# Optimization experiments

Hardware: AMD Instinct MI355X
Metric: run time of the kernel (lower is better)

The kernel has to match this reference:

```python
import jax, jax.numpy as jnp
import numpy as np

N, ID, OD, M, S, L = 65536, 16, 8, 1024, 8, 64


def setup_inputs() -> dict:
    key = jax.random.key(0)
    k1, k2, k3, k4, k5, k6 = jax.random.split(key, 6)
    return {
        "x": jax.random.normal(k1, (N, ID), dtype=jnp.float32),
        "inducing_locations": jax.random.uniform(k2, (M, ID), dtype=jnp.float32),
        "inducing_weights": jax.random.normal(k3, (S, OD, M), dtype=jnp.float32),
        "prior_frequency": jax.random.normal(k4, (OD, ID, L), dtype=jnp.float32),
        "prior_phase": jax.random.uniform(k5, (OD, L), dtype=jnp.float32, maxval=2 * np.pi),
        "prior_weights": jax.random.normal(k6, (S, OD, L), dtype=jnp.float32),
    }


def _rbf_matrix(x, z):
    # ExponentiatedQuadratic with amplitude=1, length_scale=1:
    # k(x,z) = exp(-0.5 * ||x - z||^2)
    x2 = jnp.sum(x * x, axis=-1)[:, None]          # [N,1]
    z2 = jnp.sum(z * z, axis=-1)[None, :]          # [1,M]
    sq = jnp.maximum(x2 + z2 - 2.0 * (x @ z.T), 0.0)
    return jnp.exp(-0.5 * sq)                      # [N,M]


def reference(x, inducing_locations, inducing_weights, prior_frequency, prior_phase, prior_weights):
    # ---- prior (random Fourier features) ----
    # spectral_weights for unit RBF: outer_weights = ones((OD,L)), inner_weights = ones((ID,))
    # rescaled_x = x / 1 = x
    # basis_fn_inner_prod: [OD, N, L]
    inner = jnp.einsum('ni,oil->onl', x, prior_frequency)
    basis_fn = jnp.cos(inner + prior_phase[:, None, :])              # [OD,N,L]
    basis_weight = jnp.sqrt(2.0 / prior_frequency.shape[-1]) * prior_weights  # [S,OD,L]
    f_prior = jnp.einsum('onl,sol->son', basis_fn, basis_weight)     # [S,OD,N]

    # ---- data term (kernel matrix + matvec) ----
    K = _rbf_matrix(x, inducing_locations)                           # [N,M]
    f_data = jnp.einsum('nm,som->son', K, inducing_weights)          # [S,OD,N]

    return f_prior + f_data
```

## Files before the change

kernel.cpp:

```cpp
#include <hip/hip_runtime.h>
#include <hip/hip_bf16.h>

#define N_PTS 65536
#define LOG2E 1.4426950408889634f
#define INV2PI 0.15915494309189535f

typedef __attribute__((ext_vector_type(8))) short short8;
typedef __attribute__((ext_vector_type(4))) short short4v;
typedef __attribute__((ext_vector_type(4))) float float4v;

#if __has_builtin(__builtin_amdgcn_exp2f)
#define EXP2F(x) __builtin_amdgcn_exp2f(x)
#else
#define EXP2F(x) exp2f(x)
#endif

#if __has_builtin(__builtin_amdgcn_cosf) && __has_builtin(__builtin_amdgcn_fractf)
#define COSR(x) __builtin_amdgcn_cosf(__builtin_amdgcn_fractf(x))
#else
#define COSR(x) __cosf((x) * 6.283185307179586f)
#endif

__device__ __forceinline__ short f2b(float f) {
    __hip_bfloat16 h = __float2bfloat16(f);
    return *(short*)&h;
}
__device__ __forceinline__ float b2f(short s) {
    __hip_bfloat16 h = *(__hip_bfloat16*)&s;
    return __bfloat162float(h);
}

#if __has_builtin(__builtin_amdgcn_mfma_f32_16x16x16bf16_1k)
#define HAVE_MFMA16 1
typedef short4v pafrag;
__device__ __forceinline__ float4v pmfma(pafrag a, pafrag b, float4v c) {
    return __builtin_amdgcn_mfma_f32_16x16x16bf16_1k(a, b, c, 0, 0, 0);
}
#else
#define HAVE_MFMA16 0
typedef short8 pafrag;
__device__ __forceinline__ float4v pmfma(pafrag a, pafrag b, float4v c) {
    return __builtin_amdgcn_mfma_f32_16x16x32_bf16(a, b, c, 0, 0, 0);
}
#endif

__device__ __forceinline__ pafrag ldrow(const short* base, int row16, int q, int c) {
#if HAVE_MFMA16
    return *(const pafrag*)(base + (size_t)(row16 + c) * 16 + 4 * q);
#else
    pafrag v = (pafrag)0;
    if (q < 2) v = *(const pafrag*)(base + (size_t)(row16 + c) * 16 + 8 * q);
    return v;
#endif
}
__device__ __forceinline__ pafrag mkxfrag(const float* x, size_t row, int q) {
#if HAVE_MFMA16
    float4v v = *(const float4v*)(x + row * 16 + 4 * q);
    pafrag a;
    a[0] = f2b(v.x); a[1] = f2b(v.y); a[2] = f2b(v.z); a[3] = f2b(v.w);
    return a;
#else
    pafrag a = (pafrag)0;
    if (q < 2) {
        const float4v* xp = (const float4v*)(x + row * 16 + 8 * q);
        float4v v0 = xp[0], v1 = xp[1];
        a[0] = f2b(v0.x); a[1] = f2b(v0.y); a[2] = f2b(v0.z); a[3] = f2b(v0.w);
        a[4] = f2b(v1.x); a[5] = f2b(v1.y); a[6] = f2b(v1.z); a[7] = f2b(v1.w);
    }
    return a;
#endif
}

__device__ __forceinline__ int permrow(int p) {
    return ((p & 12) << 1) + (p & 3) + ((p >> 4) << 2);
}

__global__ __launch_bounds__(256) void prep_kernel(
    const float* __restrict__ z, const float* __restrict__ W,
    const float* __restrict__ F, const float* __restrict__ pw,
    const float* __restrict__ ph,
    short* __restrict__ zb, short* __restrict__ FbB,
    short* __restrict__ BWd, short* __restrict__ Wtb,
    float* __restrict__ nz2P, float* __restrict__ phP)
{
    int t = blockIdx.x * 256 + threadIdx.x;
    if (t < 16384) {
        int row = t >> 4, i = t & 15;
        int src = (row & ~31) + permrow(row & 31);
        zb[t] = f2b(LOG2E * z[src * 16 + i]);
    } else if (t < 17408) {
        int m = t - 16384;
        int src = (m & ~31) + permrow(m & 31);
        const float4v* zp = (const float4v*)(z + (size_t)src * 16);
        float s = 0.f;
        #pragma unroll
        for (int k = 0; k < 4; k++) {
            float4v v = zp[k];
            float a0 = b2f(f2b(v.x)), a1 = b2f(f2b(v.y));
            float a2 = b2f(f2b(v.z)), a3 = b2f(f2b(v.w));
            s += a0 * a0 + a1 * a1 + a2 * a2 + a3 * a3;
        }
        nz2P[m] = -(0.5f * LOG2E * s);
    } else if (t < 25600) {
        int p = t - 17408;
        int row = p >> 4, i = p & 15;
        int srow = (row & ~31) + permrow(row & 31);
        int o = srow >> 6, l = srow & 63;
        FbB[p] = f2b(INV2PI * F[o * 1024 + i * 64 + l]);
    } else if (t < 58368) {
        int p = t - 25600;
        int so = p >> 9, ol = p & 511, o = ol >> 6;
        float v = ((so & 7) == o) ? 0.17677669529663687f * pw[so * 64 + (ol & 63)] : 0.f;
        BWd[p] = f2b(v);
    } else if (t < 123904) {
        int p = t - 58368;
        Wtb[p] = f2b(W[p]);
    } else {
        int j = t - 123904;
        int sj = (j & ~31) + permrow(j & 31);
        phP[j] = INV2PI * ph[sj];
    }
}

__global__ __launch_bounds__(256, 4) void fused_kernel(
    const float* __restrict__ x,
    const short* __restrict__ zb, const short* __restrict__ FbB,
    const short* __restrict__ BWd, const short* __restrict__ Wtb,
    const float* __restrict__ nz2P, const float* __restrict__ phP,
    float* __restrict__ out)
{
    __shared__ float x2c[64];
    __shared__ __align__(16) float rbufA[64 * 68];
    __shared__ __align__(16) float rbufB[64 * 68];

    const int tid = threadIdx.x;
    const int lane = tid & 63, w = tid >> 6;
    const int q = lane >> 4, c = lane & 15;
    const int n0 = blockIdx.x * 64;

    if (tid < 64) {
        float s = 0.f;
        const float4v* xr = (const float4v*)(x + (size_t)(n0 + tid) * 16);
        #pragma unroll
        for (int k = 0; k < 4; k++) {
            float4v v = xr[k];
            float a0 = b2f(f2b(v.x)), a1 = b2f(f2b(v.y));
            float a2 = b2f(f2b(v.z)), a3 = b2f(f2b(v.w));
            s += a0 * a0 + a1 * a1 + a2 * a2 + a3 * a3;
        }
        x2c[tid] = 0.5f * LOG2E * s;
    }

    pafrag ax[4];
    #pragma unroll
    for (int nt = 0; nt < 4; nt++)
        ax[nt] = mkxfrag(x, (size_t)(n0 + nt * 16 + c), q);

    float4v acc[4][4];
    #pragma unroll
    for (int a = 0; a < 4; a++)
        #pragma unroll
        for (int nt = 0; nt < 4; nt++) acc[a][nt] = (float4v)(0.f);

    __syncthreads();

    const int mbase = w * 256;
    #pragma unroll 2
    for (int mb = 0; mb < 8; mb++) {
        const int m0 = mbase + mb * 32;
        pafrag bzA = ldrow(zb, m0, q, c);
        pafrag bzB = ldrow(zb, m0 + 16, q, c);
        float4v c0A = *(const float4v*)(nz2P + m0 + 4 * q);
        float4v c0B = *(const float4v*)(nz2P + m0 + 16 + 4 * q);
        short8 aw0 = *(const short8*)(Wtb + (size_t)(0 * 16 + c) * 1024 + m0 + q * 8);
        short8 aw1 = *(const short8*)(Wtb + (size_t)(1 * 16 + c) * 1024 + m0 + q * 8);
        short8 aw2 = *(const short8*)(Wtb + (size_t)(2 * 16 + c) * 1024 + m0 + q * 8);
        short8 aw3 = *(const short8*)(Wtb + (size_t)(3 * 16 + c) * 1024 + m0 + q * 8);
        #pragma unroll
        for (int nt = 0; nt < 4; nt++) {
            float4v dA = pmfma(bzA, ax[nt], c0A);
            float4v dB = pmfma(bzB, ax[nt], c0B);
            short8 pb;
            pb[0] = f2b(EXP2F(dA[0])); pb[1] = f2b(EXP2F(dA[1]));
            pb[2] = f2b(EXP2F(dA[2])); pb[3] = f2b(EXP2F(dA[3]));
            pb[4] = f2b(EXP2F(dB[0])); pb[5] = f2b(EXP2F(dB[1]));
            pb[6] = f2b(EXP2F(dB[2])); pb[7] = f2b(EXP2F(dB[3]));
            acc[0][nt] = __builtin_amdgcn_mfma_f32_16x16x32_bf16(aw0, pb, acc[0][nt], 0, 0, 0);
            acc[1][nt] = __builtin_amdgcn_mfma_f32_16x16x32_bf16(aw1, pb, acc[1][nt], 0, 0, 0);
            acc[2][nt] = __builtin_amdgcn_mfma_f32_16x16x32_bf16(aw2, pb, acc[2][nt], 0, 0, 0);
            acc[3][nt] = __builtin_amdgcn_mfma_f32_16x16x32_bf16(aw3, pb, acc[3][nt], 0, 0, 0);
        }
    }

    #pragma unroll
    for (int nt = 0; nt < 4; nt++) {
        float sxv = EXP2F(-x2c[nt * 16 + c]);
        #pragma unroll
        for (int a = 0; a < 4; a++) acc[a][nt] *= sxv;
    }

    const int lbase = w * 128;
    #pragma unroll 2
    for (int lb = 0; lb < 4; lb++) {
        const int l0 = lbase + lb * 32;
        pafrag bfA = ldrow(FbB, l0, q, c);
        pafrag bfB = ldrow(FbB, l0 + 16, q, c);
        float4v c0A = *(const float4v*)(phP + l0 + 4 * q);
        float4v c0B = *(const float4v*)(phP + l0 + 16 + 4 * q);
        short8 aw0 = *(const short8*)(BWd + (size_t)(0 * 16 + c) * 512 + l0 + q * 8);
        short8 aw1 = *(const short8*)(BWd + (size_t)(1 * 16 + c) * 512 + l0 + q * 8);
        short8 aw2 = *(const short8*)(BWd + (size_t)(2 * 16 + c) * 512 + l0 + q * 8);
        short8 aw3 = *(const short8*)(BWd + (size_t)(3 * 16 + c) * 512 + l0 + q * 8);
        #pragma unroll
        for (int nt = 0; nt < 4; nt++) {
            float4v dA = pmfma(bfA, ax[nt], c0A);
            float4v dB = pmfma(bfB, ax[nt], c0B);
            short8 pb;
            pb[0] = f2b(COSR(dA[0])); pb[1] = f2b(COSR(dA[1]));
            pb[2] = f2b(COSR(dA[2])); pb[3] = f2b(COSR(dA[3]));
            pb[4] = f2b(COSR(dB[0])); pb[5] = f2b(COSR(dB[1]));
            pb[6] = f2b(COSR(dB[2])); pb[7] = f2b(COSR(dB[3]));
            acc[0][nt] = __builtin_amdgcn_mfma_f32_16x16x32_bf16(aw0, pb, acc[0][nt], 0, 0, 0);
            acc[1][nt] = __builtin_amdgcn_mfma_f32_16x16x32_bf16(aw1, pb, acc[1][nt], 0, 0, 0);
            acc[2][nt] = __builtin_amdgcn_mfma_f32_16x16x32_bf16(aw2, pb, acc[2][nt], 0, 0, 0);
            acc[3][nt] = __builtin_amdgcn_mfma_f32_16x16x32_bf16(aw3, pb, acc[3][nt], 0, 0, 0);
        }
    }

    __syncthreads();
    if (w & 1) {
        float* rb = (w == 1) ? rbufA : rbufB;
        #pragma unroll
        for (int a = 0; a < 4; a++)
            #pragma unroll
            for (int nt = 0; nt < 4; nt++)
                #pragma unroll
                for (int r = 0; r < 4; r++)
                    rb[(a * 16 + 4 * q + r) * 68 + nt * 16 + c] = acc[a][nt][r];
    }
    __syncthreads();
    if (!(w & 1)) {
        float* rb = (w == 0) ? rbufA : rbufB;
        #pragma unroll
        for (int a = 0; a < 4; a++)
            #pragma unroll
            for (int nt = 0; nt < 4; nt++)
                #pragma unroll
                for (int r = 0; r < 4; r++) {
                    int idx = (a * 16 + 4 * q + r) * 68 + nt * 16 + c;
                    rb[idx] += acc[a][nt][r];
                }
    }
    __syncthreads();
    #pragma unroll
    for (int k = 0; k < 16; k++) {
        int idx = k * 256 + tid;
        int row = idx >> 6, nn = idx & 63;
        out[(size_t)row * N_PTS + n0 + nn] = rbufA[row * 68 + nn] + rbufB[row * 68 + nn];
    }
}

extern "C" void kernel_launch(void* const* d_in, const int* in_sizes, int n_in,
                              void* d_out, int out_size, void* d_ws, size_t ws_size,
                              hipStream_t stream) {
    const float* x  = (const float*)d_in[0];
    const float* z  = (const float*)d_in[1];
    const float* W  = (const float*)d_in[2];
    const float* F  = (const float*)d_in[3];
    const float* ph = (const float*)d_in[4];
    const float* pw = (const float*)d_in[5];
    float* out = (float*)d_out;

    char* ws = (char*)d_ws;
    short* zb   = (short*)(ws);
    short* FbB  = (short*)(ws + 32768);
    short* BWd  = (short*)(ws + 49152);
    short* Wtb  = (short*)(ws + 114688);
    float* nz2P = (float*)(ws + 245760);
    float* phP  = (float*)(ws + 249856);

    prep_kernel<<<486, 256, 0, stream>>>(z, W, F, pw, ph, zb, FbB, BWd, Wtb, nz2P, phP);
    fused_kernel<<<1024, 256, 0, stream>>>(x, zb, FbB, BWd, Wtb, nz2P, phP, out);
}
```

Baseline: 107.5 us.

## Give each wave its own 16 points over the full M and L range

Before, four waves shared 64 points and split the M/L reduction, then combined partial sums through LDS. Now each wave of a 128-thread block owns 16 points and loops over all of M and L. That removes the LDS reduction and its barriers, and it writes output straight from registers. It also swaps the bf16 conversion for a manual pack with round-half-up. In exchange, each wave reloads the weight fragments four times as often per point, does less MFMA work per load, and the output stores become less coalesced.

```diff
diff --git a/kernel.cpp b/kernel.cpp
--- a/kernel.cpp
+++ b/kernel.cpp
@@ -8,6 +8,7 @@
 typedef __attribute__((ext_vector_type(8))) short short8;
 typedef __attribute__((ext_vector_type(4))) short short4v;
 typedef __attribute__((ext_vector_type(4))) float float4v;
+typedef __attribute__((ext_vector_type(4))) unsigned int uint4v;
 
 #if __has_builtin(__builtin_amdgcn_exp2f)
 #define EXP2F(x) __builtin_amdgcn_exp2f(x)
@@ -28,6 +29,12 @@
 __device__ __forceinline__ float b2f(short s) {
     __hip_bfloat16 h = *(__hip_bfloat16*)&s;
     return __bfloat162float(h);
+}
+
+__device__ __forceinline__ unsigned int pkbf(float a, float b) {
+    unsigned int ua = __builtin_bit_cast(unsigned int, a) + 0x8000u;
+    unsigned int ub = __builtin_bit_cast(unsigned int, b) + 0x8000u;
+    return (ua >> 16) | (ub & 0xFFFF0000u);
 }
 
 #if __has_builtin(__builtin_amdgcn_mfma_f32_16x16x16bf16_1k)
@@ -122,23 +129,22 @@
     }
 }
 
-__global__ __launch_bounds__(256, 4) void fused_kernel(
+__global__ __launch_bounds__(128, 5) void fused_kernel(
     const float* __restrict__ x,
     const short* __restrict__ zb, const short* __restrict__ FbB,
     const short* __restrict__ BWd, const short* __restrict__ Wtb,
     const float* __restrict__ nz2P, const float* __restrict__ phP,
     float* __restrict__ out)
 {
-    __shared__ float x2c[64];
-    __shared__ __align__(16) float rbufA[64 * 68];
-    __shared__ __align__(16) float rbufB[64 * 68];
+    __shared__ float x2c[32];
 
     const int tid = threadIdx.x;
     const int lane = tid & 63, w = tid >> 6;
     const int q = lane >> 4, c = lane & 15;
-    const int n0 = blockIdx.x * 64;
-
-    if (tid < 64) {
+    const int n0 = blockIdx.x * 32;
+    const int nw = n0 + w * 16;
+
+    if (tid < 32) {
         float s = 0.f;
         const float4v* xr = (const float4v*)(x + (size_t)(n0 + tid) * 16);
         #pragma unroll
@@ -151,23 +157,17 @@
         x2c[tid] = 0.5f * LOG2E * s;
     }
 
-    pafrag ax[4];
+    pafrag ax = mkxfrag(x, (size_t)(nw + c), q);
+
+    float4v acc[4];
     #pragma unroll
-    for (int nt = 0; nt < 4; nt++)
-        ax[nt] = mkxfrag(x, (size_t)(n0 + nt * 16 + c), q);
-
-    float4v acc[4][4];
-    #pragma unroll
-    for (int a = 0; a < 4; a++)
-        #pragma unroll
-        for (int nt = 0; nt < 4; nt++) acc[a][nt] = (float4v)(0.f);
+    for (int a = 0; a < 4; a++) acc[a] = (float4v)(0.f);
 
     __syncthreads();
 
-    const int mbase = w * 256;
     #pragma unroll 2
-    for (int mb = 0; mb < 8; mb++) {
-        const int m0 = mbase + mb * 32;
+    for (int mb = 0; mb < 32; mb++) {
+        const int m0 = mb * 32;
         pafrag bzA = ldrow(zb, m0, q, c);
         pafrag bzB = ldrow(zb, m0 + 16, q, c);
         float4v c0A = *(const float4v*)(nz2P + m0 + 4 * q);
@@ -176,33 +176,29 @@
         short8 aw1 = *(const short8*)(Wtb + (size_t)(1 * 16 + c) * 1024 + m0 + q * 8);
         short8 aw2 = *(const short8*)(Wtb + (size_t)(2 * 16 + c) * 1024 + m0 + q * 8);
         short8 aw3 = *(const short8*)(Wtb + (size_t)(3 * 16 + c) * 1024 + m0 + q * 8);
-        #pragma unroll
-        for (int nt = 0; nt < 4; nt++) {
-            float4v dA = pmfma(bzA, ax[nt], c0A);
-            float4v dB = pmfma(bzB, ax[nt], c0B);
-            short8 pb;
-            pb[0] = f2b(EXP2F(dA[0])); pb[1] = f2b(EXP2F(dA[1]));
-            pb[2] = f2b(EXP2F(dA[2])); pb[3] = f2b(EXP2F(dA[3]));
-            pb[4] = f2b(EXP2F(dB[0])); pb[5] = f2b(EXP2F(dB[1]));
-            pb[6] = f2b(EXP2F(dB[2])); pb[7] = f2b(EXP2F(dB[3]));
-            acc[0][nt] = __builtin_amdgcn_mfma_f32_16x16x32_bf16(aw0, pb, acc[0][nt], 0, 0, 0);
-            acc[1][nt] = __builtin_amdgcn_mfma_f32_16x16x32_bf16(aw1, pb, acc[1][nt], 0, 0, 0);
-            acc[2][nt] = __builtin_amdgcn_mfma_f32_16x16x32_bf16(aw2, pb, acc[2][nt], 0, 0, 0);
-            acc[3][nt] = __builtin_amdgcn_mfma_f32_16x16x32_bf16(aw3, pb, acc[3][nt], 0, 0, 0);
-        }
-    }
-
-    #pragma unroll
-    for (int nt = 0; nt < 4; nt++) {
-        float sxv = EXP2F(-x2c[nt * 16 + c]);
-        #pragma unroll
-        for (int a = 0; a < 4; a++) acc[a][nt] *= sxv;
-    }
-
-    const int lbase = w * 128;
+        float4v dA = pmfma(bzA, ax, c0A);
+        float4v dB = pmfma(bzB, ax, c0B);
+        uint4v u;
+        u[0] = pkbf(EXP2F(dA[0]), EXP2F(dA[1]));
+        u[1] = pkbf(EXP2F(dA[2]), EXP2F(dA[3]));
+        u[2] = pkbf(EXP2F(dB[0]), EXP2F(dB[1]));
+        u[3] = pkbf(EXP2F(dB[2]), EXP2F(dB[3]));
+        short8 pb = __builtin_bit_cast(short8, u);
+        acc[0] = __builtin_amdgcn_mfma_f32_16x16x32_bf16(aw0, pb, acc[0], 0, 0, 0);
+        acc[1] = __builtin_amdgcn_mfma_f32_16x16x32_bf16(aw1, pb, acc[1], 0, 0, 0);
+        acc[2] = __builtin_amdgcn_mfma_f32_16x16x32_bf16(aw2, pb, acc[2], 0, 0, 0);
+        acc[3] = __builtin_amdgcn_mfma_f32_16x16x32_bf16(aw3, pb, acc[3], 0, 0, 0);
+    }
+
+    {
+        float sxv = EXP2F(-x2c[w * 16 + c]);
+        #pragma unroll
+        for (int a = 0; a < 4; a++) acc[a] *= sxv;
+    }
+
     #pragma unroll 2
-    for (int lb = 0; lb < 4; lb++) {
-        const int l0 = lbase + lb * 32;
+    for (int lb = 0; lb < 16; lb++) {
+        const int l0 = lb * 32;
         pafrag bfA = ldrow(FbB, l0, q, c);
         pafrag bfB = ldrow(FbB, l0 + 16, q, c);
         float4v c0A = *(const float4v*)(phP + l0 + 4 * q);
@@ -211,52 +207,26 @@
         short8 aw1 = *(const short8*)(BWd + (size_t)(1 * 16 + c) * 512 + l0 + q * 8);
         short8 aw2 = *(const short8*)(BWd + (size_t)(2 * 16 + c) * 512 + l0 + q * 8);
         short8 aw3 = *(const short8*)(BWd + (size_t)(3 * 16 + c) * 512 + l0 + q * 8);
-        #pragma unroll
-        for (int nt = 0; nt < 4; nt++) {
-            float4v dA = pmfma(bfA, ax[nt], c0A);
-            float4v dB = pmfma(bfB, ax[nt], c0B);
-            short8 pb;
-            pb[0] = f2b(COSR(dA[0])); pb[1] = f2b(COSR(dA[1]));
-            pb[2] = f2b(COSR(dA[2])); pb[3] = f2b(COSR(dA[3]));
-            pb[4] = f2b(COSR(dB[0])); pb[5] = f2b(COSR(dB[1]));
-            pb[6] = f2b(COSR(dB[2])); pb[7] = f2b(COSR(dB[3]));
-            acc[0][nt] = __builtin_amdgcn_mfma_f32_16x16x32_bf16(aw0, pb, acc[0][nt], 0, 0, 0);
-            acc[1][nt] = __builtin_amdgcn_mfma_f32_16x16x32_bf16(aw1, pb, acc[1][nt], 0, 0, 0);
-            acc[2][nt] = __builtin_amdgcn_mfma_f32_16x16x32_bf16(aw2, pb, acc[2][nt], 0, 0, 0);
-            acc[3][nt] = __builtin_amdgcn_mfma_f32_16x16x32_bf16(aw3, pb, acc[3][nt], 0, 0, 0);
+        float4v dA = pmfma(bfA, ax, c0A);
+        float4v dB = pmfma(bfB, ax, c0B);
+        uint4v u;
+        u[0] = pkbf(COSR(dA[0]), COSR(dA[1]));
+        u[1] = pkbf(COSR(dA[2]), COSR(dA[3]));
+        u[2] = pkbf(COSR(dB[0]), COSR(dB[1]));
+        u[3] = pkbf(COSR(dB[2]), COSR(dB[3]));
+        short8 pb = __builtin_bit_cast(short8, u);
+        acc[0] = __builtin_amdgcn_mfma_f32_16x16x32_bf16(aw0, pb, acc[0], 0, 0, 0);
+        acc[1] = __builtin_amdgcn_mfma_f32_16x16x32_bf16(aw1, pb, acc[1], 0, 0, 0);
+        acc[2] = __builtin_amdgcn_mfma_f32_16x16x32_bf16(aw2, pb, acc[2], 0, 0, 0);
+        acc[3] = __builtin_amdgcn_mfma_f32_16x16x32_bf16(aw3, pb, acc[3], 0, 0, 0);
+    }
+
+    #pragma unroll
+    for (int a = 0; a < 4; a++) {
+        #pragma unroll
+        for (int r = 0; r < 4; r++) {
+            out[(size_t)(a * 16 + 4 * q + r) * N_PTS + nw + c] = acc[a][r];
         }
-    }
-
-    __syncthreads();
-    if (w & 1) {
-        float* rb = (w == 1) ? rbufA : rbufB;
-        #pragma unroll
-        for (int a = 0; a < 4; a++)
-            #pragma unroll
-            for (int nt = 0; nt < 4; nt++)
-                #pragma unroll
-                for (int r = 0; r < 4; r++)
-                    rb[(a * 16 + 4 * q + r) * 68 + nt * 16 + c] = acc[a][nt][r];
-    }
-    __syncthreads();
-    if (!(w & 1)) {
-        float* rb = (w == 0) ? rbufA : rbufB;
-        #pragma unroll
-        for (int a = 0; a < 4; a++)
-            #pragma unroll
-            for (int nt = 0; nt < 4; nt++)
-                #pragma unroll
-                for (int r = 0; r < 4; r++) {
-                    int idx = (a * 16 + 4 * q + r) * 68 + nt * 16 + c;
-                    rb[idx] += acc[a][nt][r];
-                }
-    }
-    __syncthreads();
-    #pragma unroll
-    for (int k = 0; k < 16; k++) {
-        int idx = k * 256 + tid;
-        int row = idx >> 6, nn = idx & 63;
-        out[(size_t)row * N_PTS + n0 + nn] = rbufA[row * 68 + nn] + rbufB[row * 68 + nn];
     }
 }
 
@@ -280,5 +250,5 @@
     float* phP  = (float*)(ws + 249856);
 
     prep_kernel<<<486, 256, 0, stream>>>(z, W, F, pw, ph, zb, FbB, BWd, Wtb, nz2P, phP);
-    fused_kernel<<<1024, 256, 0, stream>>>(x, zb, FbB, BWd, Wtb, nz2P, phP, out);
-}
+    fused_kernel<<<2048, 128, 0, stream>>>(x, zb, FbB, BWd, Wtb, nz2P, phP, out);
+}
```

Result: slower. 179.2 us (+66.7%).

## Pack bf16 conversion via bit tricks, fully unroll loops, raise MFMA priority

Applied to the files above, without the earlier changes.

Replaces the per-element __float2bfloat16 conversion (round-to-nearest-even with NaN handling) with a cheap round-half-up bit-add that packs two bf16 values into each 32-bit word. Both the RBF and cosine feature loops are now fully unrolled, and s_setprio is raised around each MFMA burst so waves interleave transcendental/VALU work with matrix work. The aim is to cut VALU instruction count in the conversion-heavy inner loops. The trade-offs are slightly different rounding (ties round up, no NaN special-casing) and higher register pressure from full unrolling.

```diff
diff --git a/kernel.cpp b/kernel.cpp
--- a/kernel.cpp
+++ b/kernel.cpp
@@ -8,6 +8,7 @@
 typedef __attribute__((ext_vector_type(8))) short short8;
 typedef __attribute__((ext_vector_type(4))) short short4v;
 typedef __attribute__((ext_vector_type(4))) float float4v;
+typedef __attribute__((ext_vector_type(4))) unsigned int uint4v;
 
 #if __has_builtin(__builtin_amdgcn_exp2f)
 #define EXP2F(x) __builtin_amdgcn_exp2f(x)
@@ -28,6 +29,12 @@
 __device__ __forceinline__ float b2f(short s) {
     __hip_bfloat16 h = *(__hip_bfloat16*)&s;
     return __bfloat162float(h);
+}
+
+__device__ __forceinline__ unsigned int pkbf(float a, float b) {
+    unsigned int ua = __builtin_bit_cast(unsigned int, a) + 0x8000u;
+    unsigned int ub = __builtin_bit_cast(unsigned int, b) + 0x8000u;
+    return (ua >> 16) | (ub & 0xFFFF0000u);
 }
 
 #if __has_builtin(__builtin_amdgcn_mfma_f32_16x16x16bf16_1k)
@@ -165,7 +172,7 @@
     __syncthreads();
 
     const int mbase = w * 256;
-    #pragma unroll 2
+    #pragma unroll
     for (int mb = 0; mb < 8; mb++) {
         const int m0 = mbase + mb * 32;
         pafrag bzA = ldrow(zb, m0, q, c);
@@ -180,15 +187,18 @@
         for (int nt = 0; nt < 4; nt++) {
             float4v dA = pmfma(bzA, ax[nt], c0A);
             float4v dB = pmfma(bzB, ax[nt], c0B);
-            short8 pb;
-            pb[0] = f2b(EXP2F(dA[0])); pb[1] = f2b(EXP2F(dA[1]));
-            pb[2] = f2b(EXP2F(dA[2])); pb[3] = f2b(EXP2F(dA[3]));
-            pb[4] = f2b(EXP2F(dB[0])); pb[5] = f2b(EXP2F(dB[1]));
-            pb[6] = f2b(EXP2F(dB[2])); pb[7] = f2b(EXP2F(dB[3]));
+            uint4v u;
+            u[0] = pkbf(EXP2F(dA[0]), EXP2F(dA[1]));
+            u[1] = pkbf(EXP2F(dA[2]), EXP2F(dA[3]));
+            u[2] = pkbf(EXP2F(dB[0]), EXP2F(dB[1]));
+            u[3] = pkbf(EXP2F(dB[2]), EXP2F(dB[3]));
+            short8 pb = __builtin_bit_cast(short8, u);
+            __builtin_amdgcn_s_setprio(1);
             acc[0][nt] = __builtin_amdgcn_mfma_f32_16x16x32_bf16(aw0, pb, acc[0][nt], 0, 0, 0);
             acc[1][nt] = __builtin_amdgcn_mfma_f32_16x16x32_bf16(aw1, pb, acc[1][nt], 0, 0, 0);
             acc[2][nt] = __builtin_amdgcn_mfma_f32_16x16x32_bf16(aw2, pb, acc[2][nt], 0, 0, 0);
             acc[3][nt] = __builtin_amdgcn_mfma_f32_16x16x32_bf16(aw3, pb, acc[3][nt], 0, 0, 0);
+            __builtin_amdgcn_s_setprio(0);
         }
     }
 
@@ -200,7 +210,7 @@
     }
 
     const int lbase = w * 128;
-    #pragma unroll 2
+    #pragma unroll
     for (int lb = 0; lb < 4; lb++) {
         const int l0 = lbase + lb * 32;
         pafrag bfA = ldrow(FbB, l0, q, c);
@@ -215,15 +225,18 @@
         for (int nt = 0; nt < 4; nt++) {
             float4v dA = pmfma(bfA, ax[nt], c0A);
             float4v dB = pmfma(bfB, ax[nt], c0B);
-            short8 pb;
-            pb[0] = f2b(COSR(dA[0])); pb[1] = f2b(COSR(dA[1]));
-            pb[2] = f2b(COSR(dA[2])); pb[3] = f2b(COSR(dA[3]));
-            pb[4] = f2b(COSR(dB[0])); pb[5] = f2b(COSR(dB[1]));
-            pb[6] = f2b(COSR(dB[2])); pb[7] = f2b(COSR(dB[3]));
+            uint4v u;
+            u[0] = pkbf(COSR(dA[0]), COSR(dA[1]));
+            u[1] = pkbf(COSR(dA[2]), COSR(dA[3]));
+            u[2] = pkbf(COSR(dB[0]), COSR(dB[1]));
+            u[3] = pkbf(COSR(dB[2]), COSR(dB[3]));
+            short8 pb = __builtin_bit_cast(short8, u);
+            __builtin_amdgcn_s_setprio(1);
             acc[0][nt] = __builtin_amdgcn_mfma_f32_16x16x32_bf16(aw0, pb, acc[0][nt], 0, 0, 0);
             acc[1][nt] = __builtin_amdgcn_mfma_f32_16x16x32_bf16(aw1, pb, acc[1][nt], 0, 0, 0);
             acc[2][nt] = __builtin_amdgcn_mfma_f32_16x16x32_bf16(aw2, pb, acc[2][nt], 0, 0, 0);
             acc[3][nt] = __builtin_amdgcn_mfma_f32_16x16x32_bf16(aw3, pb, acc[3][nt], 0, 0, 0);
+            __builtin_amdgcn_s_setprio(0);
         }
     }
 
```

Result: slower. 116.2 us (+8.1%).
